# Kernel tuning notes

Measured on AMD Instinct MI355X. Metric: run time of the kernel, lower is better.

Reference implementation:

```python
import jax, jax.numpy as jnp
import numpy as np

BLOCK = 32          # QLinearLPBQ block_size
W_BITS = 4          # low-precision blockwise weight quantization
ACT_BITS = 16       # ActivationQDQ(bits=16)


def act_qdq(x):
    # per-tensor symmetric 16-bit fake quant-dequant (dynamic absmax scale)
    qmax = 2.0 ** (ACT_BITS - 1) - 1.0  # 32767
    scale = jnp.maximum(jnp.max(jnp.abs(x)) / qmax, 1e-12)
    return jnp.clip(jnp.round(x / scale), -qmax - 1.0, qmax) * scale


def fixed_qdq_u16(x):
    # FixedActivationQDQ: scale = 1/65536, zero_point = 0, unsigned 16-bit grid
    scale = 1.0 / 65536.0
    return jnp.clip(jnp.round(x / scale), 0.0, 65535.0) * scale


def lpbq_dequant(w):
    # blockwise (per output row, per 32-wide input block) 4-bit fake quant-dequant
    O, I = w.shape
    qmax = 2.0 ** (W_BITS - 1) - 1.0  # 7
    wb = w.reshape(O, I // BLOCK, BLOCK)
    s = jnp.maximum(jnp.max(jnp.abs(wb), axis=-1, keepdims=True) / qmax, 1e-12)
    wq = jnp.clip(jnp.round(wb / s), -qmax - 1.0, qmax) * s
    return wq.reshape(O, I)


def setup_inputs() -> dict:
    key = jax.random.key(0)
    k1, k2, k3, k4 = jax.random.split(key, 4)
    B, S, H, I = 2, 4096, 1024, 3072
    x = jax.random.normal(k1, (B, S, H), jnp.float32)
    w_gate = jax.random.normal(k2, (I, H), jnp.float32) * 0.02
    w_up = jax.random.normal(k3, (I, H), jnp.float32) * 0.02
    w_down = jax.random.normal(k4, (H, I), jnp.float32) * 0.02
    return {"x": x, "w_gate": w_gate, "w_up": w_up, "w_down": w_down}


def reference(x, w_gate, w_up, w_down):
    # x: [B, S, H]
    x = act_qdq(x)                                        # up_proj_input_qdq
    up = act_qdq(x @ lpbq_dequant(w_up).T)                # up_proj + output qdq -> [B,S,I]
    gate = act_qdq(x @ lpbq_dequant(w_gate).T)            # gate_proj + output qdq
    sig = fixed_qdq_u16(jax.nn.sigmoid(gate))             # sigmoid on fixed u16 grid
    gate = act_qdq(gate * sig)                            # SiLU (x*sigmoid) + qdq
    o = act_qdq(gate * up)                                # down_proj_input_qdq
    return o @ lpbq_dequant(w_down).T                     # [B, S, H]
```

## Files before the change

### kernel.cpp

```cpp
#include <hip/hip_runtime.h>
#include <hip/hip_bf16.h>
#include <stdint.h>


#define M_ROWS 8192
#define H_DIM 1024
#define I_DIM 3072

typedef unsigned short u16;
typedef unsigned int u32;
typedef __attribute__((ext_vector_type(8))) short bf16x8;
typedef __attribute__((ext_vector_type(4))) float f32x4;

__device__ __forceinline__ float bf2f(u16 v) { return __uint_as_float(((u32)v) << 16); }
__device__ __forceinline__ u16 f2bf(float f) {
  u32 u = __float_as_uint(f);
  u32 r = (u + 0x7fffu + ((u >> 16) & 1u)) >> 16;
  return (u16)r;
}
__device__ __forceinline__ float qdq16i(float x, float inv, float s) {
  float q = rintf(x * inv);
  q = fminf(fmaxf(q, -32768.f), 32767.f);
  return q * s;
}
__device__ __forceinline__ float sigq(float g) {
  float sig = __builtin_amdgcn_rcpf(1.f + __expf(-g));
  return fminf(fmaxf(rintf(sig * 65536.f), 0.f), 65535.f) * (1.f / 65536.f);
}

__device__ __forceinline__ float scale_read(const u32* __restrict__ scal, int s) {
  u32 m = 0;
#pragma unroll
  for (int j = 0; j < 16; ++j) m = max(m, scal[j * 16 + s]);
  return fmaxf(__uint_as_float(m) / 32767.f, 1e-12f);
}

__device__ __forceinline__ void load_lds16(const u16* g, u16* lds) {
  __builtin_amdgcn_global_load_lds(
      (const __attribute__((address_space(1))) u32*)g,
      (__attribute__((address_space(3))) u32*)lds, 16, 0, 0);
}

__device__ __forceinline__ void block_amax_atomic(float mx, u32* scal, int s) {
#pragma unroll
  for (int off = 32; off; off >>= 1) mx = fmaxf(mx, __shfl_xor(mx, off));
  __shared__ float red[4];
  const int lane = threadIdx.x & 63, wave = threadIdx.x >> 6;
  if (lane == 0) red[wave] = mx;
  __syncthreads();
  if (threadIdx.x == 0) {
    float m = fmaxf(fmaxf(red[0], red[1]), fmaxf(red[2], red[3]));
    atomicMax(scal + (blockIdx.x & 15) * 16 + s, __float_as_uint(m));
  }
}

__device__ __forceinline__ void block_amax4(float a, float b, float c, float d,
                                            u32* __restrict__ scal) {
#pragma unroll
  for (int off = 32; off; off >>= 1) {
    a = fmaxf(a, __shfl_xor(a, off));
    b = fmaxf(b, __shfl_xor(b, off));
    c = fmaxf(c, __shfl_xor(c, off));
    d = fmaxf(d, __shfl_xor(d, off));
  }
  __shared__ float red4[4][4];
  const int lane = threadIdx.x & 63, wave = threadIdx.x >> 6;
  if (lane == 0) {
    red4[0][wave] = a;
    red4[1][wave] = b;
    red4[2][wave] = c;
    red4[3][wave] = d;
  }
  __syncthreads();
  if (threadIdx.x == 0) {
    u32* base = scal + (blockIdx.x & 15) * 16;
#pragma unroll
    for (int s = 0; s < 4; ++s) {
      float m = fmaxf(fmaxf(red4[s][0], red4[s][1]), fmaxf(red4[s][2], red4[s][3]));
      atomicMax(base + 1 + s, __float_as_uint(m));
    }
  }
}

template <int K>
__device__ __forceinline__ void gemm_core64(const u16* __restrict__ Ablk,
                                            const u16* __restrict__ Bblk,
                                            f32x4 acc[4][4], u16* smem) {
  u16* As = smem;
  u16* Bs = smem + 8192;
  const int tid = threadIdx.x;
  const int lane = tid & 63, wave = tid >> 6;
  const int wm = wave >> 1, wn = wave & 1;
  const int quad = lane >> 4, mrow = lane & 15;

  int goff[4], loff[4];
#pragma unroll
  for (int t = 0; t < 4; ++t) {
    const int c = tid + 256 * t;
    const int r = c >> 3, q = c & 7;
    goff[t] = r * K + ((q ^ (r & 7)) << 3);
    loff[t] = c << 3;
  }
  const int pc0 = (quad ^ (mrow & 7)) << 3;
  const int pc1 = ((quad + 4) ^ (mrow & 7)) << 3;
  int arow[4], brow[4];
#pragma unroll
  for (int i = 0; i < 4; ++i) {
    arow[i] = (wm * 64 + i * 16 + mrow) << 6;
    brow[i] = (wn * 64 + i * 16 + mrow) << 6;
  }

  for (int k0 = 0; k0 < K; k0 += 64) {
    __syncthreads();
#pragma unroll
    for (int t = 0; t < 4; ++t) {
      load_lds16(Ablk + k0 + goff[t], As + loff[t]);
      load_lds16(Bblk + k0 + goff[t], Bs + loff[t]);
    }
    __syncthreads();
#pragma unroll
    for (int kk = 0; kk < 2; ++kk) {
      const int pc = kk ? pc1 : pc0;
      bf16x8 af[4];
#pragma unroll
      for (int t = 0; t < 4; ++t) af[t] = *(const bf16x8*)&As[arow[t] + pc];
#pragma unroll
      for (int j = 0; j < 4; ++j) {
        bf16x8 b = *(const bf16x8*)&Bs[brow[j] + pc];
#pragma unroll
        for (int i = 0; i < 4; ++i)
          acc[i][j] = __builtin_amdgcn_mfma_f32_16x16x32_bf16(af[i], b, acc[i][j], 0, 0, 0);
      }
    }
  }
}

__global__ void __launch_bounds__(256, 2) kgemm1(const u16* __restrict__ xq,
                                                 const u16* __restrict__ wcat,
                                                 u16* __restrict__ up, u16* __restrict__ gh,
                                                 u32* __restrict__ scal) {
  __shared__ __align__(16) u16 smem[24576];
  u16* As = smem;
  u16* Bus = smem + 8192;
  u16* Bgs = smem + 16384;
  const int tileN = blockIdx.x * 128;
  const int tileM = blockIdx.y * 128;
  const int tid = threadIdx.x;
  const int lane = tid & 63, wave = tid >> 6;
  const int wm = wave >> 1, wn = wave & 1;
  const int quad = lane >> 4, mrow = lane & 15;

  const u16* Ablk = xq + (size_t)tileM * H_DIM;
  const u16* Bublk = wcat + (size_t)tileN * H_DIM;
  const u16* Bgblk = wcat + (size_t)(I_DIM + tileN) * H_DIM;

  int goff[4], loff[4];
#pragma unroll
  for (int t = 0; t < 4; ++t) {
    const int c = tid + 256 * t;
    const int r = c >> 3, q = c & 7;
    goff[t] = r * H_DIM + ((q ^ (r & 7)) << 3);
    loff[t] = c << 3;
  }
  const int pc0 = (quad ^ (mrow & 7)) << 3;
  const int pc1 = ((quad + 4) ^ (mrow & 7)) << 3;
  int arow[4], brow[4];
#pragma unroll
  for (int i = 0; i < 4; ++i) {
    arow[i] = (wm * 64 + i * 16 + mrow) << 6;
    brow[i] = (wn * 64 + i * 16 + mrow) << 6;
  }

  f32x4 accg[4][4], accu[4][4];
#pragma unroll
  for (int i = 0; i < 4; ++i)
#pragma unroll
    for (int j = 0; j < 4; ++j) {
      accg[i][j] = (f32x4){0.f, 0.f, 0.f, 0.f};
      accu[i][j] = (f32x4){0.f, 0.f, 0.f, 0.f};
    }

  for (int k0 = 0; k0 < H_DIM; k0 += 64) {
    __syncthreads();
#pragma unroll
    for (int t = 0; t < 4; ++t) {
      load_lds16(Ablk + k0 + goff[t], As + loff[t]);
      load_lds16(Bublk + k0 + goff[t], Bus + loff[t]);
      load_lds16(Bgblk + k0 + goff[t], Bgs + loff[t]);
    }
    __syncthreads();
#pragma unroll
    for (int kk = 0; kk < 2; ++kk) {
      const int pc = kk ? pc1 : pc0;
      bf16x8 af[4];
#pragma unroll
      for (int t = 0; t < 4; ++t) af[t] = *(const bf16x8*)&As[arow[t] + pc];
#pragma unroll
      for (int j = 0; j < 4; ++j) {
        bf16x8 b = *(const bf16x8*)&Bus[brow[j] + pc];
#pragma unroll
        for (int i = 0; i < 4; ++i)
          accu[i][j] = __builtin_amdgcn_mfma_f32_16x16x32_bf16(af[i], b, accu[i][j], 0, 0, 0);
      }
#pragma unroll
      for (int j = 0; j < 4; ++j) {
        bf16x8 b = *(const bf16x8*)&Bgs[brow[j] + pc];
#pragma unroll
        for (int i = 0; i < 4; ++i)
          accg[i][j] = __builtin_amdgcn_mfma_f32_16x16x32_bf16(af[i], b, accg[i][j], 0, 0, 0);
      }
    }
  }

  const int rb = (lane >> 4) * 4, cb = lane & 15;
  const int erow = lane >> 2, echk = lane & 3;
  u16* gstage = smem + wave * 1152;
  u16* ustage = smem + 8192 + wave * 1152;
  const u16* grb = gstage + erow * 72;
  const u16* urb = ustage + erow * 72;
  float mxg = 0.f, mxu = 0.f, mxh = 0.f, mxo = 0.f;
#pragma unroll
  for (int i = 0; i < 4; ++i) {
    __syncthreads();
#pragma unroll
    for (int j = 0; j < 4; ++j)
#pragma unroll
      for (int r = 0; r < 4; ++r) {
        float g = accg[i][j][r];
        float u = accu[i][j][r];
        mxg = fmaxf(mxg, fabsf(g));
        mxu = fmaxf(mxu, fabsf(u));
        float ha = g * sigq(g);
        mxh = fmaxf(mxh, fabsf(ha));
        mxo = fmaxf(mxo, fabsf(ha * u));
        gstage[(rb + r) * 72 + j * 16 + cb] = f2bf(g);
        ustage[(rb + r) * 72 + j * 16 + cb] = f2bf(u);
      }
    __syncthreads();
    uint4 g0 = *(const uint4*)(grb + echk * 8);
    uint4 g1 = *(const uint4*)(grb + (echk + 4) * 8);
    uint4 u0 = *(const uint4*)(urb + echk * 8);
    uint4 u1 = *(const uint4*)(urb + (echk + 4) * 8);
    size_t grow = (size_t)(tileM + wm * 64 + i * 16 + erow) * I_DIM + (tileN + wn * 64);
    *(uint4*)(gh + grow + echk * 8) = g0;
    *(uint4*)(gh + grow + (echk + 4) * 8) = g1;
    *(uint4*)(up + grow + echk * 8) = u0;
    *(uint4*)(up + grow + (echk + 4) * 8) = u1;
  }
  block_amax4(mxu, mxg, mxh, mxo, scal);
}

__global__ void __launch_bounds__(256) kgemm2(const u16* __restrict__ oq,
                                              const u16* __restrict__ wdq,
                                              float* __restrict__ out) {
  __shared__ __align__(16) u16 smem[16384];
  const int tileN = blockIdx.x * 128;
  const int tileM = blockIdx.y * 128;
  f32x4 acc[4][4];
#pragma unroll
  for (int i = 0; i < 4; ++i)
#pragma unroll
    for (int j = 0; j < 4; ++j) acc[i][j] = (f32x4){0.f, 0.f, 0.f, 0.f};
  gemm_core64<I_DIM>(oq + (size_t)tileM * I_DIM, wdq + (size_t)tileN * I_DIM, acc, smem);

  const int lane = threadIdx.x & 63, wave = threadIdx.x >> 6;
  const int wm = wave >> 1, wn = wave & 1;
  const int rb = (lane >> 4) * 4, cb = lane & 15;
#pragma unroll
  for (int i = 0; i < 4; ++i) {
#pragma unroll
    for (int j = 0; j < 4; ++j) {
      size_t base = (size_t)(tileM + wm * 64 + i * 16 + rb) * H_DIM +
                    (size_t)(tileN + wn * 64 + j * 16 + cb);
#pragma unroll
      for (int r = 0; r < 4; ++r) out[base + (size_t)r * H_DIM] = acc[i][j][r];
    }
  }
}

__global__ void __launch_bounds__(256) kprep(const float* __restrict__ x,
                                             const float* __restrict__ wu,
                                             const float* __restrict__ wg,
                                             const float* __restrict__ wdn,
                                             u16* __restrict__ wcat, u16* __restrict__ wdq,
                                             u32* __restrict__ scal) {
  if (blockIdx.x < 1024) {
    const float4* x4 = (const float4*)x;
    const int n4 = (M_ROWS * H_DIM) / 4;
    float mx = 0.f;
    for (int i = blockIdx.x * 256 + threadIdx.x; i < n4; i += 1024 * 256) {
      float4 v = x4[i];
      mx = fmaxf(fmaxf(fabsf(v.x), fabsf(v.y)), fmaxf(fmaxf(fabsf(v.z), fabsf(v.w)), mx));
    }
    block_amax_atomic(mx, scal, 0);
    return;
  }
  const int gid = (blockIdx.x - 1024) * 256 + threadIdx.x;
  const int unit = gid >> 3, l8 = gid & 7;
  const float* src;
  u16* dst;
  int u;
  if (unit < 98304)       { src = wu;  dst = wcat;            u = unit; }
  else if (unit < 196608) { src = wg;  dst = wcat + 3145728;  u = unit - 98304; }
  else                    { src = wdn; dst = wdq;             u = unit - 196608; }
  const size_t off = (size_t)u * 32 + (size_t)l8 * 4;
  float4 v = *(const float4*)(src + off);
  float m = fmaxf(fmaxf(fabsf(v.x), fabsf(v.y)), fmaxf(fabsf(v.z), fabsf(v.w)));
  m = fmaxf(m, __shfl_xor(m, 1));
  m = fmaxf(m, __shfl_xor(m, 2));
  m = fmaxf(m, __shfl_xor(m, 4));
  const float s = fmaxf(m / 7.0f, 1e-12f);
  const float inv = 1.0f / s;
  float vv[4] = {v.x, v.y, v.z, v.w};
  u16 o[4];
#pragma unroll
  for (int e = 0; e < 4; ++e) {
    float q = rintf(vv[e] * inv);
    q = fminf(fmaxf(q, -8.f), 7.f);
    o[e] = f2bf(q * s);
  }
  *(ushort4*)(dst + off) = make_ushort4(o[0], o[1], o[2], o[3]);
}

__global__ void __launch_bounds__(256) kqdqx(const float4* __restrict__ x,
                                             ushort4* __restrict__ xq,
                                             const u32* __restrict__ scal) {
  const float s = scale_read(scal, 0);
  const float inv = 1.0f / s;
  const int i = blockIdx.x * 256 + threadIdx.x;
  float4 v = x[i];
  ushort4 o;
  o.x = f2bf(qdq16i(v.x, inv, s));
  o.y = f2bf(qdq16i(v.y, inv, s));
  o.z = f2bf(qdq16i(v.z, inv, s));
  o.w = f2bf(qdq16i(v.w, inv, s));
  xq[i] = o;
}

#define GH4 ((M_ROWS * I_DIM) / 8)
#define EW_BLOCKS 2048

__global__ void __launch_bounds__(256) kmulo(uint4* __restrict__ gh, const uint4* __restrict__ up,
                                             u32* __restrict__ scal) {
  const float sg = scale_read(scal, 2), ig = 1.0f / sg;
  const float sh = scale_read(scal, 3), ih = 1.0f / sh;
  const float su = scale_read(scal, 1), iu = 1.0f / su;
  const float so = scale_read(scal, 4), io = 1.0f / so;
  for (int i = blockIdx.x * 256 + threadIdx.x; i < GH4; i += EW_BLOCKS * 256) {
    union { uint4 v; u16 us[8]; } a, b;
    a.v = gh[i];
    b.v = up[i];
#pragma unroll
    for (int e = 0; e < 8; ++e) {
      float g = qdq16i(bf2f(a.us[e]), ig, sg);
      float h = g * sigq(g);
      float o = qdq16i(h, ih, sh) * qdq16i(bf2f(b.us[e]), iu, su);
      a.us[e] = f2bf(qdq16i(o, io, so));
    }
    gh[i] = a.v;
  }
}

extern "C" void kernel_launch(void* const* d_in, const int* in_sizes, int n_in,
                              void* d_out, int out_size, void* d_ws, size_t ws_size,
                              hipStream_t stream) {
  (void)in_sizes; (void)n_in; (void)out_size; (void)ws_size;
  const float* x   = (const float*)d_in[0];
  const float* wg  = (const float*)d_in[1];
  const float* wu  = (const float*)d_in[2];
  const float* wdn = (const float*)d_in[3];
  float* out = (float*)d_out;
  char* ws = (char*)d_ws;

  u32* scal = (u32*)ws;
  u16* xq   = (u16*)(ws + 1024);
  u16* wcat = xq + (size_t)M_ROWS * H_DIM;
  u16* wdq  = wcat + (size_t)2 * I_DIM * H_DIM;
  u16* up   = wdq + (size_t)H_DIM * I_DIM;
  u16* gh   = up + (size_t)M_ROWS * I_DIM;

  hipMemsetAsync(scal, 0, 1024, stream);
  kprep<<<1024 + 9216, 256, 0, stream>>>(x, wu, wg, wdn, wcat, wdq, scal);
  kqdqx<<<(M_ROWS * H_DIM) / 4 / 256, 256, 0, stream>>>((const float4*)x, (ushort4*)xq, scal);
  kgemm1<<<dim3(24, 64), 256, 0, stream>>>(xq, wcat, up, gh, scal);
  kmulo<<<EW_BLOCKS, 256, 0, stream>>>((uint4*)gh, (const uint4*)up, scal);
  kgemm2<<<dim3(8, 64), 256, 0, stream>>>(gh, wdq, out);
}
```

Baseline: 323.3 us.

## Double-buffer LDS and enlarge GEMM tiles to 256x128 with 512-thread blocks

Both GEMM kernels move from 128x128 tiles with 256 threads to 256x128 tiles with 8 waves. The LDS is double-buffered so the next K-slice's global-to-LDS loads are issued before computing on the current one, leaving one barrier per iteration. This is meant to hide global load latency behind MFMA work and to reuse each B tile across twice as many rows. In exchange, LDS use rises to 128KB for kgemm1 and 96KB for kgemm2, which likely limits each CU to one block and leaves fewer blocks to balance the grid. The block amax reduction is widened to cover 8 waves.

```diff
diff --git a/kernel.cpp b/kernel.cpp
--- a/kernel.cpp
+++ b/kernel.cpp
@@ -54,8 +54,8 @@
   }
 }
 
-__device__ __forceinline__ void block_amax4(float a, float b, float c, float d,
-                                            u32* __restrict__ scal) {
+__device__ __forceinline__ void block_amax4_8w(float a, float b, float c, float d,
+                                               u32* __restrict__ scal) {
 #pragma unroll
   for (int off = 32; off; off >>= 1) {
     a = fmaxf(a, __shfl_xor(a, off));
@@ -63,7 +63,7 @@
     c = fmaxf(c, __shfl_xor(c, off));
     d = fmaxf(d, __shfl_xor(d, off));
   }
-  __shared__ float red4[4][4];
+  __shared__ float red4[4][8];
   const int lane = threadIdx.x & 63, wave = threadIdx.x >> 6;
   if (lane == 0) {
     red4[0][wave] = a;
@@ -76,30 +76,44 @@
     u32* base = scal + (blockIdx.x & 15) * 16;
 #pragma unroll
     for (int s = 0; s < 4; ++s) {
-      float m = fmaxf(fmaxf(red4[s][0], red4[s][1]), fmaxf(red4[s][2], red4[s][3]));
+      float m = 0.f;
+#pragma unroll
+      for (int w = 0; w < 8; ++w) m = fmaxf(m, red4[s][w]);
       atomicMax(base + 1 + s, __float_as_uint(m));
     }
   }
 }
 
-template <int K>
-__device__ __forceinline__ void gemm_core64(const u16* __restrict__ Ablk,
-                                            const u16* __restrict__ Bblk,
-                                            f32x4 acc[4][4], u16* smem) {
-  u16* As = smem;
-  u16* Bs = smem + 8192;
+__global__ void __launch_bounds__(512, 2) kgemm1(const u16* __restrict__ xq,
+                                                 const u16* __restrict__ wcat,
+                                                 u16* __restrict__ up, u16* __restrict__ gh,
+                                                 u32* __restrict__ scal) {
+  __shared__ __align__(16) u16 smem[65536];
+  const int tileN = blockIdx.x * 128;
+  const int tileM = blockIdx.y * 256;
   const int tid = threadIdx.x;
   const int lane = tid & 63, wave = tid >> 6;
   const int wm = wave >> 1, wn = wave & 1;
   const int quad = lane >> 4, mrow = lane & 15;
 
-  int goff[4], loff[4];
+  const u16* Ablk = xq + (size_t)tileM * H_DIM;
+  const u16* Bublk = wcat + (size_t)tileN * H_DIM;
+  const u16* Bgblk = wcat + (size_t)(I_DIM + tileN) * H_DIM;
+
+  int goffA[4], loffA[4], goffB[2], loffB[2];
 #pragma unroll
   for (int t = 0; t < 4; ++t) {
-    const int c = tid + 256 * t;
+    const int c = tid + 512 * t;
     const int r = c >> 3, q = c & 7;
-    goff[t] = r * K + ((q ^ (r & 7)) << 3);
-    loff[t] = c << 3;
+    goffA[t] = r * H_DIM + ((q ^ (r & 7)) << 3);
+    loffA[t] = c << 3;
+  }
+#pragma unroll
+  for (int t = 0; t < 2; ++t) {
+    const int c = tid + 512 * t;
+    const int r = c >> 3, q = c & 7;
+    goffB[t] = r * H_DIM + ((q ^ (r & 7)) << 3);
+    loffB[t] = c << 3;
   }
   const int pc0 = (quad ^ (mrow & 7)) << 3;
   const int pc1 = ((quad + 4) ^ (mrow & 7)) << 3;
@@ -110,14 +124,41 @@
     brow[i] = (wn * 64 + i * 16 + mrow) << 6;
   }
 
-  for (int k0 = 0; k0 < K; k0 += 64) {
-    __syncthreads();
-#pragma unroll
-    for (int t = 0; t < 4; ++t) {
-      load_lds16(Ablk + k0 + goff[t], As + loff[t]);
-      load_lds16(Bblk + k0 + goff[t], Bs + loff[t]);
-    }
-    __syncthreads();
+  f32x4 accg[4][4], accu[4][4];
+#pragma unroll
+  for (int i = 0; i < 4; ++i)
+#pragma unroll
+    for (int j = 0; j < 4; ++j) {
+      accg[i][j] = (f32x4){0.f, 0.f, 0.f, 0.f};
+      accu[i][j] = (f32x4){0.f, 0.f, 0.f, 0.f};
+    }
+
+  {
+    u16* d = smem;
+#pragma unroll
+    for (int t = 0; t < 4; ++t) load_lds16(Ablk + goffA[t], d + loffA[t]);
+#pragma unroll
+    for (int t = 0; t < 2; ++t) load_lds16(Bublk + goffB[t], d + 16384 + loffB[t]);
+#pragma unroll
+    for (int t = 0; t < 2; ++t) load_lds16(Bgblk + goffB[t], d + 24576 + loffB[t]);
+  }
+  __syncthreads();
+
+  int cur = 0;
+  for (int k0 = 0; k0 < H_DIM; k0 += 64) {
+    if (k0 + 64 < H_DIM) {
+      u16* d = smem + (cur ^ 1) * 32768;
+      const int kn = k0 + 64;
+#pragma unroll
+      for (int t = 0; t < 4; ++t) load_lds16(Ablk + kn + goffA[t], d + loffA[t]);
+#pragma unroll
+      for (int t = 0; t < 2; ++t) load_lds16(Bublk + kn + goffB[t], d + 16384 + loffB[t]);
+#pragma unroll
+      for (int t = 0; t < 2; ++t) load_lds16(Bgblk + kn + goffB[t], d + 24576 + loffB[t]);
+    }
+    const u16* As = smem + cur * 32768;
+    const u16* Bus = As + 16384;
+    const u16* Bgs = As + 24576;
 #pragma unroll
     for (int kk = 0; kk < 2; ++kk) {
       const int pc = kk ? pc1 : pc0;
@@ -126,77 +167,6 @@
       for (int t = 0; t < 4; ++t) af[t] = *(const bf16x8*)&As[arow[t] + pc];
 #pragma unroll
       for (int j = 0; j < 4; ++j) {
-        bf16x8 b = *(const bf16x8*)&Bs[brow[j] + pc];
-#pragma unroll
-        for (int i = 0; i < 4; ++i)
-          acc[i][j] = __builtin_amdgcn_mfma_f32_16x16x32_bf16(af[i], b, acc[i][j], 0, 0, 0);
-      }
-    }
-  }
-}
-
-__global__ void __launch_bounds__(256, 2) kgemm1(const u16* __restrict__ xq,
-                                                 const u16* __restrict__ wcat,
-                                                 u16* __restrict__ up, u16* __restrict__ gh,
-                                                 u32* __restrict__ scal) {
-  __shared__ __align__(16) u16 smem[24576];
-  u16* As = smem;
-  u16* Bus = smem + 8192;
-  u16* Bgs = smem + 16384;
-  const int tileN = blockIdx.x * 128;
-  const int tileM = blockIdx.y * 128;
-  const int tid = threadIdx.x;
-  const int lane = tid & 63, wave = tid >> 6;
-  const int wm = wave >> 1, wn = wave & 1;
-  const int quad = lane >> 4, mrow = lane & 15;
-
-  const u16* Ablk = xq + (size_t)tileM * H_DIM;
-  const u16* Bublk = wcat + (size_t)tileN * H_DIM;
-  const u16* Bgblk = wcat + (size_t)(I_DIM + tileN) * H_DIM;
-
-  int goff[4], loff[4];
-#pragma unroll
-  for (int t = 0; t < 4; ++t) {
-    const int c = tid + 256 * t;
-    const int r = c >> 3, q = c & 7;
-    goff[t] = r * H_DIM + ((q ^ (r & 7)) << 3);
-    loff[t] = c << 3;
-  }
-  const int pc0 = (quad ^ (mrow & 7)) << 3;
-  const int pc1 = ((quad + 4) ^ (mrow & 7)) << 3;
-  int arow[4], brow[4];
-#pragma unroll
-  for (int i = 0; i < 4; ++i) {
-    arow[i] = (wm * 64 + i * 16 + mrow) << 6;
-    brow[i] = (wn * 64 + i * 16 + mrow) << 6;
-  }
-
-  f32x4 accg[4][4], accu[4][4];
-#pragma unroll
-  for (int i = 0; i < 4; ++i)
-#pragma unroll
-    for (int j = 0; j < 4; ++j) {
-      accg[i][j] = (f32x4){0.f, 0.f, 0.f, 0.f};
-      accu[i][j] = (f32x4){0.f, 0.f, 0.f, 0.f};
-    }
-
-  for (int k0 = 0; k0 < H_DIM; k0 += 64) {
-    __syncthreads();
-#pragma unroll
-    for (int t = 0; t < 4; ++t) {
-      load_lds16(Ablk + k0 + goff[t], As + loff[t]);
-      load_lds16(Bublk + k0 + goff[t], Bus + loff[t]);
-      load_lds16(Bgblk + k0 + goff[t], Bgs + loff[t]);
-    }
-    __syncthreads();
-#pragma unroll
-    for (int kk = 0; kk < 2; ++kk) {
-      const int pc = kk ? pc1 : pc0;
-      bf16x8 af[4];
-#pragma unroll
-      for (int t = 0; t < 4; ++t) af[t] = *(const bf16x8*)&As[arow[t] + pc];
-#pragma unroll
-      for (int j = 0; j < 4; ++j) {
         bf16x8 b = *(const bf16x8*)&Bus[brow[j] + pc];
 #pragma unroll
         for (int i = 0; i < 4; ++i)
@@ -210,12 +180,14 @@
           accg[i][j] = __builtin_amdgcn_mfma_f32_16x16x32_bf16(af[i], b, accg[i][j], 0, 0, 0);
       }
     }
+    __syncthreads();
+    cur ^= 1;
   }
 
   const int rb = (lane >> 4) * 4, cb = lane & 15;
   const int erow = lane >> 2, echk = lane & 3;
   u16* gstage = smem + wave * 1152;
-  u16* ustage = smem + 8192 + wave * 1152;
+  u16* ustage = smem + 16384 + wave * 1152;
   const u16* grb = gstage + erow * 72;
   const u16* urb = ustage + erow * 72;
   float mxg = 0.f, mxu = 0.f, mxh = 0.f, mxo = 0.f;
@@ -247,24 +219,92 @@
     *(uint4*)(up + grow + echk * 8) = u0;
     *(uint4*)(up + grow + (echk + 4) * 8) = u1;
   }
-  block_amax4(mxu, mxg, mxh, mxo, scal);
-}
-
-__global__ void __launch_bounds__(256) kgemm2(const u16* __restrict__ oq,
-                                              const u16* __restrict__ wdq,
-                                              float* __restrict__ out) {
-  __shared__ __align__(16) u16 smem[16384];
+  block_amax4_8w(mxu, mxg, mxh, mxo, scal);
+}
+
+__global__ void __launch_bounds__(512, 2) kgemm2(const u16* __restrict__ oq,
+                                                 const u16* __restrict__ wdq,
+                                                 float* __restrict__ out) {
+  __shared__ __align__(16) u16 smem[49152];
   const int tileN = blockIdx.x * 128;
-  const int tileM = blockIdx.y * 128;
+  const int tileM = blockIdx.y * 256;
+  const int tid = threadIdx.x;
+  const int lane = tid & 63, wave = tid >> 6;
+  const int wm = wave >> 1, wn = wave & 1;
+  const int quad = lane >> 4, mrow = lane & 15;
+
+  const u16* Ablk = oq + (size_t)tileM * I_DIM;
+  const u16* Bblk = wdq + (size_t)tileN * I_DIM;
+
+  int goffA[4], loffA[4], goffB[2], loffB[2];
+#pragma unroll
+  for (int t = 0; t < 4; ++t) {
+    const int c = tid + 512 * t;
+    const int r = c >> 3, q = c & 7;
+    goffA[t] = r * I_DIM + ((q ^ (r & 7)) << 3);
+    loffA[t] = c << 3;
+  }
+#pragma unroll
+  for (int t = 0; t < 2; ++t) {
+    const int c = tid + 512 * t;
+    const int r = c >> 3, q = c & 7;
+    goffB[t] = r * I_DIM + ((q ^ (r & 7)) << 3);
+    loffB[t] = c << 3;
+  }
+  const int pc0 = (quad ^ (mrow & 7)) << 3;
+  const int pc1 = ((quad + 4) ^ (mrow & 7)) << 3;
+  int arow[4], brow[4];
+#pragma unroll
+  for (int i = 0; i < 4; ++i) {
+    arow[i] = (wm * 64 + i * 16 + mrow) << 6;
+    brow[i] = (wn * 64 + i * 16 + mrow) << 6;
+  }
+
   f32x4 acc[4][4];
 #pragma unroll
   for (int i = 0; i < 4; ++i)
 #pragma unroll
     for (int j = 0; j < 4; ++j) acc[i][j] = (f32x4){0.f, 0.f, 0.f, 0.f};
-  gemm_core64<I_DIM>(oq + (size_t)tileM * I_DIM, wdq + (size_t)tileN * I_DIM, acc, smem);
-
-  const int lane = threadIdx.x & 63, wave = threadIdx.x >> 6;
-  const int wm = wave >> 1, wn = wave & 1;
+
+  {
+    u16* d = smem;
+#pragma unroll
+    for (int t = 0; t < 4; ++t) load_lds16(Ablk + goffA[t], d + loffA[t]);
+#pragma unroll
+    for (int t = 0; t < 2; ++t) load_lds16(Bblk + goffB[t], d + 16384 + loffB[t]);
+  }
+  __syncthreads();
+
+  int cur = 0;
+  for (int k0 = 0; k0 < I_DIM; k0 += 64) {
+    if (k0 + 64 < I_DIM) {
+      u16* d = smem + (cur ^ 1) * 24576;
+      const int kn = k0 + 64;
+#pragma unroll
+      for (int t = 0; t < 4; ++t) load_lds16(Ablk + kn + goffA[t], d + loffA[t]);
+#pragma unroll
+      for (int t = 0; t < 2; ++t) load_lds16(Bblk + kn + goffB[t], d + 16384 + loffB[t]);
+    }
+    const u16* As = smem + cur * 24576;
+    const u16* Bs = As + 16384;
+#pragma unroll
+    for (int kk = 0; kk < 2; ++kk) {
+      const int pc = kk ? pc1 : pc0;
+      bf16x8 af[4];
+#pragma unroll
+      for (int t = 0; t < 4; ++t) af[t] = *(const bf16x8*)&As[arow[t] + pc];
+#pragma unroll
+      for (int j = 0; j < 4; ++j) {
+        bf16x8 b = *(const bf16x8*)&Bs[brow[j] + pc];
+#pragma unroll
+        for (int i = 0; i < 4; ++i)
+          acc[i][j] = __builtin_amdgcn_mfma_f32_16x16x32_bf16(af[i], b, acc[i][j], 0, 0, 0);
+      }
+    }
+    __syncthreads();
+    cur ^= 1;
+  }
+
   const int rb = (lane >> 4) * 4, cb = lane & 15;
 #pragma unroll
   for (int i = 0; i < 4; ++i) {
@@ -382,7 +422,7 @@
   hipMemsetAsync(scal, 0, 1024, stream);
   kprep<<<1024 + 9216, 256, 0, stream>>>(x, wu, wg, wdn, wcat, wdq, scal);
   kqdqx<<<(M_ROWS * H_DIM) / 4 / 256, 256, 0, stream>>>((const float4*)x, (ushort4*)xq, scal);
-  kgemm1<<<dim3(24, 64), 256, 0, stream>>>(xq, wcat, up, gh, scal);
+  kgemm1<<<dim3(24, 32), 512, 0, stream>>>(xq, wcat, up, gh, scal);
   kmulo<<<EW_BLOCKS, 256, 0, stream>>>((uint4*)gh, (const uint4*)up, scal);
-  kgemm2<<<dim3(8, 64), 256, 0, stream>>>(gh, wdq, out);
-}
+  kgemm2<<<dim3(8, 32), 512, 0, stream>>>(gh, wdq, out);
+}
```

Result: no change. 322.6 us (-0.2%).

## Multi-stage prefetch pipeline with 32-wide K tiles for both GEMMs

Applied to the files above, without the earlier changes.

Both GEMM kernels now split K into 32-wide slices and keep a ring of LDS buffers, three stages for gemm1 and four for gemm2. Async global-to-LDS loads are issued ahead and waited on with explicit vmcnt counts, so memory latency overlaps MFMA work instead of each tile being loaded and fenced by two full syncthreads. The swizzle is adapted to 32-element rows, and gemm2 gets launch bounds for two blocks per CU. This costs more LDS per block and relies on hand-tuned vmcnt values matching the number of loads issued per stage.

```diff
diff --git a/kernel.cpp b/kernel.cpp
--- a/kernel.cpp
+++ b/kernel.cpp
@@ -11,6 +11,14 @@
 typedef unsigned int u32;
 typedef __attribute__((ext_vector_type(8))) short bf16x8;
 typedef __attribute__((ext_vector_type(4))) float f32x4;
+
+#define WAITVM(n) asm volatile("s_waitcnt vmcnt(" #n ")" ::: "memory")
+#define BAR()                                   \
+  do {                                          \
+    asm volatile("" ::: "memory");              \
+    __builtin_amdgcn_s_barrier();               \
+    asm volatile("" ::: "memory");              \
+  } while (0)
 
 __device__ __forceinline__ float bf2f(u16 v) { return __uint_as_float(((u32)v) << 16); }
 __device__ __forceinline__ u16 f2bf(float f) {
@@ -82,67 +90,11 @@
   }
 }
 
-template <int K>
-__device__ __forceinline__ void gemm_core64(const u16* __restrict__ Ablk,
-                                            const u16* __restrict__ Bblk,
-                                            f32x4 acc[4][4], u16* smem) {
-  u16* As = smem;
-  u16* Bs = smem + 8192;
-  const int tid = threadIdx.x;
-  const int lane = tid & 63, wave = tid >> 6;
-  const int wm = wave >> 1, wn = wave & 1;
-  const int quad = lane >> 4, mrow = lane & 15;
-
-  int goff[4], loff[4];
-#pragma unroll
-  for (int t = 0; t < 4; ++t) {
-    const int c = tid + 256 * t;
-    const int r = c >> 3, q = c & 7;
-    goff[t] = r * K + ((q ^ (r & 7)) << 3);
-    loff[t] = c << 3;
-  }
-  const int pc0 = (quad ^ (mrow & 7)) << 3;
-  const int pc1 = ((quad + 4) ^ (mrow & 7)) << 3;
-  int arow[4], brow[4];
-#pragma unroll
-  for (int i = 0; i < 4; ++i) {
-    arow[i] = (wm * 64 + i * 16 + mrow) << 6;
-    brow[i] = (wn * 64 + i * 16 + mrow) << 6;
-  }
-
-  for (int k0 = 0; k0 < K; k0 += 64) {
-    __syncthreads();
-#pragma unroll
-    for (int t = 0; t < 4; ++t) {
-      load_lds16(Ablk + k0 + goff[t], As + loff[t]);
-      load_lds16(Bblk + k0 + goff[t], Bs + loff[t]);
-    }
-    __syncthreads();
-#pragma unroll
-    for (int kk = 0; kk < 2; ++kk) {
-      const int pc = kk ? pc1 : pc0;
-      bf16x8 af[4];
-#pragma unroll
-      for (int t = 0; t < 4; ++t) af[t] = *(const bf16x8*)&As[arow[t] + pc];
-#pragma unroll
-      for (int j = 0; j < 4; ++j) {
-        bf16x8 b = *(const bf16x8*)&Bs[brow[j] + pc];
-#pragma unroll
-        for (int i = 0; i < 4; ++i)
-          acc[i][j] = __builtin_amdgcn_mfma_f32_16x16x32_bf16(af[i], b, acc[i][j], 0, 0, 0);
-      }
-    }
-  }
-}
-
 __global__ void __launch_bounds__(256, 2) kgemm1(const u16* __restrict__ xq,
                                                  const u16* __restrict__ wcat,
                                                  u16* __restrict__ up, u16* __restrict__ gh,
                                                  u32* __restrict__ scal) {
-  __shared__ __align__(16) u16 smem[24576];
-  u16* As = smem;
-  u16* Bus = smem + 8192;
-  u16* Bgs = smem + 16384;
+  __shared__ __align__(16) u16 smem[36864];
   const int tileN = blockIdx.x * 128;
   const int tileM = blockIdx.y * 128;
   const int tid = threadIdx.x;
@@ -154,21 +106,20 @@
   const u16* Bublk = wcat + (size_t)tileN * H_DIM;
   const u16* Bgblk = wcat + (size_t)(I_DIM + tileN) * H_DIM;
 
-  int goff[4], loff[4];
-#pragma unroll
-  for (int t = 0; t < 4; ++t) {
+  int goff[2], loff[2];
+#pragma unroll
+  for (int t = 0; t < 2; ++t) {
     const int c = tid + 256 * t;
-    const int r = c >> 3, q = c & 7;
-    goff[t] = r * H_DIM + ((q ^ (r & 7)) << 3);
+    const int r = c >> 2, q = c & 3;
+    goff[t] = r * H_DIM + ((q ^ ((r >> 1) & 3)) << 3);
     loff[t] = c << 3;
   }
-  const int pc0 = (quad ^ (mrow & 7)) << 3;
-  const int pc1 = ((quad + 4) ^ (mrow & 7)) << 3;
-  int arow[4], brow[4];
+  const int pc = (quad ^ ((mrow >> 1) & 3)) << 3;
+  int aoff[4], boff[4];
 #pragma unroll
   for (int i = 0; i < 4; ++i) {
-    arow[i] = (wm * 64 + i * 16 + mrow) << 6;
-    brow[i] = (wn * 64 + i * 16 + mrow) << 6;
+    aoff[i] = (wm * 64 + i * 16 + mrow) * 32 + pc;
+    boff[i] = (wn * 64 + i * 16 + mrow) * 32 + pc;
   }
 
   f32x4 accg[4][4], accu[4][4];
@@ -180,42 +131,62 @@
       accu[i][j] = (f32x4){0.f, 0.f, 0.f, 0.f};
     }
 
-  for (int k0 = 0; k0 < H_DIM; k0 += 64) {
-    __syncthreads();
-#pragma unroll
-    for (int t = 0; t < 4; ++t) {
-      load_lds16(Ablk + k0 + goff[t], As + loff[t]);
-      load_lds16(Bublk + k0 + goff[t], Bus + loff[t]);
-      load_lds16(Bgblk + k0 + goff[t], Bgs + loff[t]);
-    }
-    __syncthreads();
-#pragma unroll
-    for (int kk = 0; kk < 2; ++kk) {
-      const int pc = kk ? pc1 : pc0;
-      bf16x8 af[4];
-#pragma unroll
-      for (int t = 0; t < 4; ++t) af[t] = *(const bf16x8*)&As[arow[t] + pc];
-#pragma unroll
-      for (int j = 0; j < 4; ++j) {
-        bf16x8 b = *(const bf16x8*)&Bus[brow[j] + pc];
-#pragma unroll
-        for (int i = 0; i < 4; ++i)
-          accu[i][j] = __builtin_amdgcn_mfma_f32_16x16x32_bf16(af[i], b, accu[i][j], 0, 0, 0);
-      }
-#pragma unroll
-      for (int j = 0; j < 4; ++j) {
-        bf16x8 b = *(const bf16x8*)&Bgs[brow[j] + pc];
-#pragma unroll
-        for (int i = 0; i < 4; ++i)
-          accg[i][j] = __builtin_amdgcn_mfma_f32_16x16x32_bf16(af[i], b, accg[i][j], 0, 0, 0);
-      }
-    }
-  }
+  auto stage = [&](int k0, int bb) {
+    u16* d = smem + bb;
+#pragma unroll
+    for (int t = 0; t < 2; ++t) load_lds16(Ablk + k0 + goff[t], d + loff[t]);
+#pragma unroll
+    for (int t = 0; t < 2; ++t) load_lds16(Bublk + k0 + goff[t], d + 4096 + loff[t]);
+#pragma unroll
+    for (int t = 0; t < 2; ++t) load_lds16(Bgblk + k0 + goff[t], d + 8192 + loff[t]);
+  };
+  auto compute = [&](int bb) {
+    const u16* As = smem + bb;
+    const u16* Bus = As + 4096;
+    const u16* Bgs = As + 8192;
+    bf16x8 af[4];
+#pragma unroll
+    for (int i = 0; i < 4; ++i) af[i] = *(const bf16x8*)&As[aoff[i]];
+#pragma unroll
+    for (int j = 0; j < 4; ++j) {
+      bf16x8 b = *(const bf16x8*)&Bus[boff[j]];
+#pragma unroll
+      for (int i = 0; i < 4; ++i)
+        accu[i][j] = __builtin_amdgcn_mfma_f32_16x16x32_bf16(af[i], b, accu[i][j], 0, 0, 0);
+    }
+#pragma unroll
+    for (int j = 0; j < 4; ++j) {
+      bf16x8 b = *(const bf16x8*)&Bgs[boff[j]];
+#pragma unroll
+      for (int i = 0; i < 4; ++i)
+        accg[i][j] = __builtin_amdgcn_mfma_f32_16x16x32_bf16(af[i], b, accg[i][j], 0, 0, 0);
+    }
+  };
+
+  stage(0, 0);
+  stage(32, 12288);
+  stage(64, 24576);
+  WAITVM(12);
+  BAR();
+
+  int bb = 0;
+#pragma unroll 1
+  for (int t = 0; t < 29; ++t) {
+    compute(bb);
+    BAR();
+    stage((t + 3) * 32, bb);
+    WAITVM(12);
+    BAR();
+    bb = (bb == 24576) ? 0 : bb + 12288;
+  }
+  compute(bb); BAR(); WAITVM(6); BAR(); bb = (bb == 24576) ? 0 : bb + 12288;
+  compute(bb); BAR(); WAITVM(0); BAR(); bb = (bb == 24576) ? 0 : bb + 12288;
+  compute(bb);
 
   const int rb = (lane >> 4) * 4, cb = lane & 15;
   const int erow = lane >> 2, echk = lane & 3;
   u16* gstage = smem + wave * 1152;
-  u16* ustage = smem + 8192 + wave * 1152;
+  u16* ustage = smem + 12288 + wave * 1152;
   const u16* grb = gstage + erow * 72;
   const u16* urb = ustage + erow * 72;
   float mxg = 0.f, mxu = 0.f, mxh = 0.f, mxo = 0.f;
@@ -250,21 +221,86 @@
   block_amax4(mxu, mxg, mxh, mxo, scal);
 }
 
-__global__ void __launch_bounds__(256) kgemm2(const u16* __restrict__ oq,
-                                              const u16* __restrict__ wdq,
-                                              float* __restrict__ out) {
-  __shared__ __align__(16) u16 smem[16384];
+__global__ void __launch_bounds__(256, 2) kgemm2(const u16* __restrict__ oq,
+                                                 const u16* __restrict__ wdq,
+                                                 float* __restrict__ out) {
+  __shared__ __align__(16) u16 smem[32768];
   const int tileN = blockIdx.x * 128;
   const int tileM = blockIdx.y * 128;
+  const int tid = threadIdx.x;
+  const int lane = tid & 63, wave = tid >> 6;
+  const int wm = wave >> 1, wn = wave & 1;
+  const int quad = lane >> 4, mrow = lane & 15;
+
+  const u16* Ablk = oq + (size_t)tileM * I_DIM;
+  const u16* Bblk = wdq + (size_t)tileN * I_DIM;
+
+  int goff[2], loff[2];
+#pragma unroll
+  for (int t = 0; t < 2; ++t) {
+    const int c = tid + 256 * t;
+    const int r = c >> 2, q = c & 3;
+    goff[t] = r * I_DIM + ((q ^ ((r >> 1) & 3)) << 3);
+    loff[t] = c << 3;
+  }
+  const int pc = (quad ^ ((mrow >> 1) & 3)) << 3;
+  int aoff[4], boff[4];
+#pragma unroll
+  for (int i = 0; i < 4; ++i) {
+    aoff[i] = (wm * 64 + i * 16 + mrow) * 32 + pc;
+    boff[i] = (wn * 64 + i * 16 + mrow) * 32 + pc;
+  }
+
   f32x4 acc[4][4];
 #pragma unroll
   for (int i = 0; i < 4; ++i)
 #pragma unroll
     for (int j = 0; j < 4; ++j) acc[i][j] = (f32x4){0.f, 0.f, 0.f, 0.f};
-  gemm_core64<I_DIM>(oq + (size_t)tileM * I_DIM, wdq + (size_t)tileN * I_DIM, acc, smem);
-
-  const int lane = threadIdx.x & 63, wave = threadIdx.x >> 6;
-  const int wm = wave >> 1, wn = wave & 1;
+
+  auto stage = [&](int k0, int bb) {
+    u16* d = smem + bb;
+#pragma unroll
+    for (int t = 0; t < 2; ++t) load_lds16(Ablk + k0 + goff[t], d + loff[t]);
+#pragma unroll
+    for (int t = 0; t < 2; ++t) load_lds16(Bblk + k0 + goff[t], d + 4096 + loff[t]);
+  };
+  auto compute = [&](int bb) {
+    const u16* As = smem + bb;
+    const u16* Bs = As + 4096;
+    bf16x8 af[4];
+#pragma unroll
+    for (int i = 0; i < 4; ++i) af[i] = *(const bf16x8*)&As[aoff[i]];
+#pragma unroll
+    for (int j = 0; j < 4; ++j) {
+      bf16x8 b = *(const bf16x8*)&Bs[boff[j]];
+#pragma unroll
+      for (int i = 0; i < 4; ++i)
+        acc[i][j] = __builtin_amdgcn_mfma_f32_16x16x32_bf16(af[i], b, acc[i][j], 0, 0, 0);
+    }
+  };
+
+  stage(0, 0);
+  stage(32, 8192);
+  stage(64, 16384);
+  stage(96, 24576);
+  WAITVM(12);
+  BAR();
+
+  int bb = 0;
+#pragma unroll 1
+  for (int t = 0; t < 92; ++t) {
+    compute(bb);
+    BAR();
+    stage((t + 4) * 32, bb);
+    WAITVM(12);
+    BAR();
+    bb = (bb + 8192) & 32767;
+  }
+  compute(bb); BAR(); WAITVM(8); BAR(); bb = (bb + 8192) & 32767;
+  compute(bb); BAR(); WAITVM(4); BAR(); bb = (bb + 8192) & 32767;
+  compute(bb); BAR(); WAITVM(0); BAR(); bb = (bb + 8192) & 32767;
+  compute(bb);
+
   const int rb = (lane >> 4) * 4, cb = lane & 15;
 #pragma unroll
   for (int i = 0; i < 4; ++i) {
```

Measured after the change: 323.1 us. About the same (-0.0%).
